# Performance work log

Hardware: AMD Instinct MI355X
Metric: run time of the kernel (lower is better)

The kernel has to match this reference:

```python
import jax, jax.numpy as jnp
import numpy as np


def setup_inputs() -> dict:
    key = jax.random.key(0)
    ks = jax.random.split(key, 8)
    B, C, H, W = 4, 512, 64, 64
    C8 = C // 8
    return {
        "x": jax.random.normal(ks[0], (B, C, H, W), dtype=jnp.float32),
        "Wq": jax.random.normal(ks[1], (C8, C), dtype=jnp.float32) * 0.02,
        "bq": jax.random.normal(ks[2], (C8,), dtype=jnp.float32) * 0.02,
        "Wk": jax.random.normal(ks[3], (C8, C), dtype=jnp.float32) * 0.02,
        "bk": jax.random.normal(ks[4], (C8,), dtype=jnp.float32) * 0.02,
        "Wv": jax.random.normal(ks[5], (C, C), dtype=jnp.float32) * 0.02,
        "bv": jax.random.normal(ks[6], (C,), dtype=jnp.float32) * 0.02,
        "gamma": jax.random.normal(ks[7], (1,), dtype=jnp.float32),
    }


def reference(x, Wq, bq, Wk, bk, Wv, bv, gamma):
    B, C, H, W = x.shape
    N = H * W
    xf = x.reshape(B, C, N)  # 1x1 conv == per-position matmul over channels
    q = jnp.einsum('oc,bcn->bno', Wq, xf) + bq  # B, N, C//8  (proj_query^T)
    k = jnp.einsum('oc,bcn->bon', Wk, xf) + bk[None, :, None]  # B, C//8, N
    v = jnp.einsum('oc,bcn->bon', Wv, xf) + bv[None, :, None]  # B, C, N
    energy = jnp.einsum('bno,bom->bnm', q, k)  # B, N, N
    attention = jax.nn.softmax(energy, axis=-1)
    # out = bmm(proj_value, attention^T): out[:, :, n] = sum_m v[:, :, m] * att[n, m]
    out = jnp.einsum('bcm,bnm->bcn', v, attention).reshape(B, C, H, W)
    return gamma[0] * out + x
```

## Files before the change

### kernel.cpp

```cpp
#include <hip/hip_runtime.h>
#include <stdint.h>


typedef unsigned short u16;
typedef unsigned char u8;
typedef __attribute__((ext_vector_type(8))) short short8;
typedef __attribute__((ext_vector_type(4))) float f32x4;
typedef __attribute__((ext_vector_type(16))) float f32x16;
typedef __attribute__((ext_vector_type(4))) int i32x4;
typedef __attribute__((ext_vector_type(8))) int i32x8;

#define ASYNC16(gp, lp)                                                        \
  __builtin_amdgcn_global_load_lds(                                            \
      (__attribute__((address_space(1))) void*)(void*)(gp),                    \
      (__attribute__((address_space(3))) void*)(lp), 16, 0, 0)

#define WAIT_VM0 0x0F70
#define WAIT_VM4 0x0F74
#define WAIT_VM8 0x0F78

#define EXP_SHIFT 5.0f
#define EXP_CAP 57000.0f

__device__ __forceinline__ u16 f2bf(float f) {
  uint32_t u = __float_as_uint(f);
  u += 0x7FFFu + ((u >> 16) & 1u);
  return (u16)(u >> 16);
}

__device__ __forceinline__ u8 f2fp8(float f) {
  f = fminf(fmaxf(f, -440.f), 440.f);
  int r = __builtin_amdgcn_cvt_pk_fp8_f32(f, f, 0, false);
  return (u8)(r & 0xFF);
}

__global__ __launch_bounds__(256) void k_transpose(const float* __restrict__ x,
                                                   u16* __restrict__ xT) {
  __shared__ float tile[32][33];
  const int b = blockIdx.z;
  const int nb = blockIdx.x * 32;
  const int cb = blockIdx.y * 32;
  const int t = threadIdx.x;
  {
    const int nl = t & 31, c0 = t >> 5;
    const float* xp = x + ((size_t)b * 512 + cb) * 4096 + nb;
#pragma unroll
    for (int i = 0; i < 4; ++i) {
      const int cl = c0 + i * 8;
      tile[cl][nl] = xp[(size_t)cl * 4096 + nl];
    }
  }
  __syncthreads();
  {
    const int cl = t & 31, n0 = t >> 5;
    u16* xtp = xT + ((size_t)b * 4096 + nb) * 512 + cb;
#pragma unroll
    for (int i = 0; i < 4; ++i) {
      const int nl = n0 + i * 8;
      xtp[(size_t)nl * 512 + cl] = f2bf(tile[cl][nl]);
    }
  }
}

__global__ __launch_bounds__(256) void k_wcast(const float* __restrict__ Wq,
                                               const float* __restrict__ Wk,
                                               const float* __restrict__ Wv,
                                               u16* __restrict__ wqk,
                                               u16* __restrict__ wv) {
  const int idx = blockIdx.x * 256 + threadIdx.x;
  if (idx < 128 * 512) {
    const int r = idx >> 9, c = idx & 511;
    const float f = (r < 64) ? Wq[r * 512 + c] : Wk[(r - 64) * 512 + c];
    wqk[idx] = f2bf(f);
  } else {
    const int j = idx - 128 * 512;
    if (j < 512 * 512) wv[j] = f2bf(Wv[j]);
  }
}

__device__ __forceinline__ void gemm_bt_tile(const u16* __restrict__ A,
                                             const u16* __restrict__ B,
                                             const int K, const int rowA0,
                                             const int colB0, u16* smem,
                                             f32x4 acc[4][4]) {
  const int t = threadIdx.x;
  const int lane = t & 63, wave = t >> 6;
  const int quad = lane >> 4, l15 = lane & 15;
  const int wr = wave >> 1, wc = wave & 1;
  u16* As = smem;
  u16* Bs = smem + 8192;
  const f32x4 zero = {0.f, 0.f, 0.f, 0.f};
#pragma unroll
  for (int i = 0; i < 4; ++i)
#pragma unroll
    for (int j = 0; j < 4; ++j) acc[i][j] = zero;

  const int srow = t >> 3;
  const int c8 = (lane & 7) ^ (lane >> 3);
  const u16* ga = A + (size_t)(rowA0 + srow) * K + c8 * 8;
  const u16* gb = B + (size_t)(colB0 + srow) * K + c8 * 8;
  char* la = (char*)As + wave * 1024;
  char* lb = (char*)Bs + wave * 1024;
  const size_t rK32 = (size_t)32 * K;

  const int sw0 = (quad) ^ (l15 & 7);
  const int sw1 = (4 + quad) ^ (l15 & 7);

  for (int k0 = 0; k0 < K; k0 += 64) {
    ASYNC16(ga + k0, la);
    ASYNC16(ga + k0 + rK32, la + 4096);
    ASYNC16(ga + k0 + 2 * rK32, la + 8192);
    ASYNC16(ga + k0 + 3 * rK32, la + 12288);
    ASYNC16(gb + k0, lb);
    ASYNC16(gb + k0 + rK32, lb + 4096);
    ASYNC16(gb + k0 + 2 * rK32, lb + 8192);
    ASYNC16(gb + k0 + 3 * rK32, lb + 12288);
    __syncthreads();
#pragma unroll
    for (int s = 0; s < 2; ++s) {
      const int sw = s ? sw1 : sw0;
      short8 a[4], b[4];
#pragma unroll
      for (int i = 0; i < 4; ++i)
        a[i] = *(const short8*)(As + (wr * 64 + i * 16 + l15) * 64 + sw * 8);
#pragma unroll
      for (int j = 0; j < 4; ++j)
        b[j] = *(const short8*)(Bs + (wc * 64 + j * 16 + l15) * 64 + sw * 8);
#pragma unroll
      for (int i = 0; i < 4; ++i)
#pragma unroll
        for (int j = 0; j < 4; ++j)
          acc[i][j] = __builtin_amdgcn_mfma_f32_16x16x32_bf16(a[i], b[j],
                                                              acc[i][j], 0, 0, 0);
    }
    __syncthreads();
  }
}

__global__ __launch_bounds__(256) void k_proj_qk(const u16* __restrict__ xT,
                                                 const u16* __restrict__ wqk,
                                                 const float* __restrict__ bq,
                                                 const float* __restrict__ bk,
                                                 u16* __restrict__ q,
                                                 u16* __restrict__ kT) {
  __shared__ u16 smem[16384];
  const int b = blockIdx.z;
  const int rowA0 = blockIdx.x * 128;
  f32x4 acc[4][4];
  gemm_bt_tile(xT + (size_t)b * 4096 * 512, wqk, 512, rowA0, 0, smem, acc);
  const int t = threadIdx.x, lane = t & 63, wave = t >> 6;
  const int quad = lane >> 4, l15 = lane & 15;
  const int wr = wave >> 1, wc = wave & 1;
#pragma unroll
  for (int j = 0; j < 4; ++j) {
    const int col = wc * 64 + j * 16 + l15;
    const float bias = (col < 64) ? bq[col] : bk[col - 64];
#pragma unroll
    for (int i = 0; i < 4; ++i) {
#pragma unroll
      for (int r = 0; r < 4; ++r) {
        const int row = rowA0 + wr * 64 + i * 16 + quad * 4 + r;
        const float val = acc[i][j][r] + bias;
        if (col < 64)
          q[((size_t)b * 4096 + row) * 64 + col] = f2bf(val);
        else
          kT[((size_t)b * 4096 + row) * 64 + (col - 64)] = f2bf(val);
      }
    }
  }
}

__global__ __launch_bounds__(256) void k_proj_v(const u16* __restrict__ wv,
                                                const u16* __restrict__ xT,
                                                const float* __restrict__ bv,
                                                u8* __restrict__ v8) {
  __shared__ u16 smem[16384];
  const int b = blockIdx.z;
  const int rowA0 = blockIdx.x * 128;
  const int colB0 = blockIdx.y * 128;
  f32x4 acc[4][4];
  gemm_bt_tile(wv, xT + (size_t)b * 4096 * 512, 512, rowA0, colB0, smem, acc);
  const int t = threadIdx.x, lane = t & 63, wave = t >> 6;
  const int quad = lane >> 4, l15 = lane & 15;
  const int wr = wave >> 1, wc = wave & 1;
#pragma unroll
  for (int i = 0; i < 4; ++i) {
#pragma unroll
    for (int r = 0; r < 4; ++r) {
      const int row = rowA0 + wr * 64 + i * 16 + quad * 4 + r;
      const float bias = bv[row];
#pragma unroll
      for (int j = 0; j < 4; ++j) {
        const int col = colB0 + wc * 64 + j * 16 + l15;
        v8[((size_t)b * 512 + row) * 4096 + col] = f2fp8(acc[i][j][r] + bias);
      }
    }
  }
}

__global__ __launch_bounds__(256, 4) void k_attn(const u16* __restrict__ q,
                                                 const u16* __restrict__ kT,
                                                 u8* __restrict__ E8,
                                                 float* __restrict__ lpart) {
  __shared__ u16 qs[4][16 * 64];
  __shared__ u16 ks[2][128 * 64];

  const int t = threadIdx.x;
  const int l = t & 63;
  const int w = t >> 6;
  const int quad = l >> 4, l15 = l & 15;
  const int c8 = (l & 7) ^ (l >> 3);
  const int r8 = l >> 3;

  const int row0 = blockIdx.x * 64 + w * 16;
  const int mpart = blockIdx.y;
  const int b = blockIdx.z;
  const int m_base = mpart * 1024;

  const u16* qg = q + ((size_t)b * 4096 + row0) * 64 + (size_t)r8 * 64 + c8 * 8;
  const u16* kg = kT + ((size_t)b * 4096 + m_base + w * 32) * 64 +
                  (size_t)r8 * 64 + c8 * 8;

  char* qls = (char*)qs + w * 2048;
  char* kls0 = (char*)ks[0] + w * 4096;
  char* kls1 = (char*)ks[1] + w * 4096;

  ASYNC16(qg, qls);
  ASYNC16(qg + 512, qls + 1024);
#pragma unroll
  for (int i = 0; i < 4; ++i) ASYNC16(kg + i * 512, kls0 + i * 1024);
#pragma unroll
  for (int i = 0; i < 4; ++i) ASYNC16(kg + 8192 + i * 512, kls1 + i * 1024);

  __builtin_amdgcn_s_waitcnt(WAIT_VM8);

  const int sw0 = quad ^ (l15 & 7);
  const int sw1 = (4 + quad) ^ (l15 & 7);
  const u16* qsw = qs[w];
  const short8 af0 = *(const short8*)(qsw + l15 * 64 + sw0 * 8);
  const short8 af1 = *(const short8*)(qsw + l15 * 64 + sw1 * 8);

  float lsum = 0.f;
  u8* Ep = E8 + ((size_t)b * 4096 + row0 + l15) * 4096 + m_base + quad * 4;
  const f32x4 zero = {0.f, 0.f, 0.f, 0.f};

  for (int it = 0; it < 8; ++it) {
    if (it < 7)
      __builtin_amdgcn_s_waitcnt(WAIT_VM4);
    else
      __builtin_amdgcn_s_waitcnt(WAIT_VM0);
    __builtin_amdgcn_s_barrier();
    asm volatile("" ::: "memory");

    const u16* kb = ks[it & 1];
    f32x4 acc[8];
#pragma unroll
    for (int j = 0; j < 8; ++j) acc[j] = zero;
    __builtin_amdgcn_s_setprio(1);
#pragma unroll
    for (int j = 0; j < 8; ++j)
      acc[j] = __builtin_amdgcn_mfma_f32_16x16x32_bf16(
          *(const short8*)(kb + (j * 16 + l15) * 64 + sw0 * 8), af0, acc[j], 0, 0, 0);
#pragma unroll
    for (int j = 0; j < 8; ++j)
      acc[j] = __builtin_amdgcn_mfma_f32_16x16x32_bf16(
          *(const short8*)(kb + (j * 16 + l15) * 64 + sw1 * 8), af1, acc[j], 0, 0, 0);
    __builtin_amdgcn_s_setprio(0);
#pragma unroll
    for (int j = 0; j < 8; ++j) {
      const float e0 = fminf(__expf(acc[j][0] - EXP_SHIFT), EXP_CAP);
      const float e1 = fminf(__expf(acc[j][1] - EXP_SHIFT), EXP_CAP);
      const float e2 = fminf(__expf(acc[j][2] - EXP_SHIFT), EXP_CAP);
      const float e3 = fminf(__expf(acc[j][3] - EXP_SHIFT), EXP_CAP);
      lsum += (e0 + e1) + (e2 + e3);
      int pk = __builtin_amdgcn_cvt_pk_bf8_f32(e0, e1, 0, false);
      pk = __builtin_amdgcn_cvt_pk_bf8_f32(e2, e3, pk, true);
      *(int*)(Ep + it * 128 + j * 16) = pk;
    }

    asm volatile("" ::: "memory");
    __builtin_amdgcn_s_barrier();
    if (it < 6) {
      char* dst = (it & 1) ? kls1 : kls0;
      const u16* src = kg + (size_t)(it + 2) * 8192;
#pragma unroll
      for (int i = 0; i < 4; ++i) ASYNC16(src + i * 512, dst + i * 1024);
    }
  }

  lsum += __shfl_xor(lsum, 16);
  lsum += __shfl_xor(lsum, 32);
  if (l < 16)
    lpart[(size_t)mpart * 16384 + (size_t)b * 4096 + row0 + l] = lsum;
}

__global__ __launch_bounds__(256) void k_lsum(const float* __restrict__ lp,
                                              float* __restrict__ ilg) {
  const int i = blockIdx.x * 256 + threadIdx.x;
  ilg[i] = 1.0f / (lp[i] + lp[16384 + i] + lp[32768 + i] + lp[49152 + i]);
}

__global__ __launch_bounds__(256) void k_pv(const u8* __restrict__ v8,
                                            const u8* __restrict__ E8,
                                            const float* __restrict__ ilg,
                                            const float* __restrict__ x,
                                            const float* __restrict__ gamma,
                                            float* __restrict__ out) {
  __shared__ u8 As[4][8192];
  __shared__ u8 Bs[4][8192];
  const int bid = blockIdx.x;
  const int xcd = bid & 7;
  const int slot = bid >> 3;
  const int c_idx = slot >> 4;
  const int group = xcd * 16 + (slot & 15);
  const int b = group >> 5;
  const int n_idx = group & 31;
  const int rowA0 = c_idx * 128;
  const int colB0 = n_idx * 128;

  const u8* Ag = v8 + (size_t)b * 512 * 4096;
  const u8* Bg = E8 + (size_t)b * 4096 * 4096;

  const int t = threadIdx.x;
  const int l = t & 63, w = t >> 6;
  const int wr = w >> 1, wc = w & 1;
  const int l31 = l & 31, h = l >> 5;

  const int srow = w * 16 + (l >> 2);
  const int ca = l & 3;
  const int f0 = (srow >> 1) & 3;
  const int f1 = ((srow + 64) >> 1) & 3;
  const u8* gA0 = Ag + (size_t)(rowA0 + srow) * 4096 + (ca ^ f0) * 16;
  const u8* gA1 = Ag + (size_t)(rowA0 + srow + 64) * 4096 + (ca ^ f1) * 16;
  const u8* gB0 = Bg + (size_t)(colB0 + srow) * 4096 + (ca ^ f0) * 16;
  const u8* gB1 = Bg + (size_t)(colB0 + srow + 64) * 4096 + (ca ^ f1) * 16;

#define STAGE_PV(bi, k0)                                                       \
  do {                                                                         \
    char* la_ = (char*)As[bi] + w * 1024;                                      \
    char* lb_ = (char*)Bs[bi] + w * 1024;                                      \
    ASYNC16(gA0 + (k0), la_);                                                  \
    ASYNC16(gA1 + (k0), la_ + 4096);                                           \
    ASYNC16(gB0 + (k0), lb_);                                                  \
    ASYNC16(gB1 + (k0), lb_ + 4096);                                           \
  } while (0)

  int rowA[2], rowB[2], sA1[2], sA2[2], sB1[2], sB2[2];
#pragma unroll
  for (int i = 0; i < 2; ++i) {
    rowA[i] = wr * 64 + i * 32 + l31;
    const int fa = (rowA[i] >> 1) & 3;
    sA1[i] = (2 * h) ^ fa;
    sA2[i] = (2 * h + 1) ^ fa;
    rowB[i] = wc * 64 + i * 32 + l31;
    const int fb = (rowB[i] >> 1) & 3;
    sB1[i] = (2 * h) ^ fb;
    sB2[i] = (2 * h + 1) ^ fb;
  }

  f32x16 acc[2][2];
#pragma unroll
  for (int i = 0; i < 2; ++i)
#pragma unroll
    for (int j = 0; j < 2; ++j)
#pragma unroll
      for (int r = 0; r < 16; ++r) acc[i][j][r] = 0.f;

  STAGE_PV(0, 0);
  STAGE_PV(1, 64);

  for (int it = 0; it < 64; ++it) {
    if (it < 63)
      __builtin_amdgcn_s_waitcnt(WAIT_VM4);
    else
      __builtin_amdgcn_s_waitcnt(WAIT_VM0);
    asm volatile("" ::: "memory");
    __builtin_amdgcn_s_barrier();
    asm volatile("" ::: "memory");
    if (it + 2 < 64) STAGE_PV((it + 2) & 3, (it + 2) * 64);

    const u8* Asb = As[it & 3];
    const u8* Bsb = Bs[it & 3];
    i32x8 a[2], bb[2];
#pragma unroll
    for (int i = 0; i < 2; ++i) {
      const u8* pa = Asb + rowA[i] * 64;
      const i32x4 lo = *(const i32x4*)(pa + sA1[i] * 16);
      const i32x4 hi = *(const i32x4*)(pa + sA2[i] * 16);
      a[i][0] = lo[0]; a[i][1] = lo[1]; a[i][2] = lo[2]; a[i][3] = lo[3];
      a[i][4] = hi[0]; a[i][5] = hi[1]; a[i][6] = hi[2]; a[i][7] = hi[3];
      const u8* pb = Bsb + rowB[i] * 64;
      const i32x4 blo = *(const i32x4*)(pb + sB1[i] * 16);
      const i32x4 bhi = *(const i32x4*)(pb + sB2[i] * 16);
      bb[i][0] = blo[0]; bb[i][1] = blo[1]; bb[i][2] = blo[2]; bb[i][3] = blo[3];
      bb[i][4] = bhi[0]; bb[i][5] = bhi[1]; bb[i][6] = bhi[2]; bb[i][7] = bhi[3];
    }
    __builtin_amdgcn_s_setprio(1);
#pragma unroll
    for (int i = 0; i < 2; ++i)
#pragma unroll
      for (int j = 0; j < 2; ++j)
        acc[i][j] = __builtin_amdgcn_mfma_scale_f32_32x32x64_f8f6f4(
            a[i], bb[j], acc[i][j], 0 , 1 , 0, 0x7F, 0, 0x7F);
    __builtin_amdgcn_s_setprio(0);
    asm volatile("" ::: "memory");
  }
#undef STAGE_PV

  const float g = gamma[0];
#pragma unroll
  for (int j = 0; j < 2; ++j) {
    const int col = colB0 + wc * 64 + j * 32 + l31;
    const float gil = g * ilg[(size_t)b * 4096 + col];
#pragma unroll
    for (int i = 0; i < 2; ++i) {
#pragma unroll
      for (int r = 0; r < 16; ++r) {
        const int rloc = (r & 3) + 8 * (r >> 2) + 4 * h;
        const int row = rowA0 + wr * 64 + i * 32 + rloc;
        const size_t idx = ((size_t)b * 512 + row) * 4096 + col;
        out[idx] = gil * acc[i][j][r] + x[idx];
      }
    }
  }
}

extern "C" void kernel_launch(void* const* d_in, const int* in_sizes, int n_in,
                              void* d_out, int out_size, void* d_ws,
                              size_t ws_size, hipStream_t stream) {
  const float* x = (const float*)d_in[0];
  const float* Wq = (const float*)d_in[1];
  const float* bq = (const float*)d_in[2];
  const float* Wk = (const float*)d_in[3];
  const float* bk = (const float*)d_in[4];
  const float* Wv = (const float*)d_in[5];
  const float* bv = (const float*)d_in[6];
  const float* gamma = (const float*)d_in[7];
  float* out = (float*)d_out;

  char* ws = (char*)d_ws;
  u16* xT = (u16*)(ws);
  u16* wqk = (u16*)(ws + 16777216);
  u16* wv = (u16*)(ws + 16908288);
  u16* qb = (u16*)(ws + 17432576);
  u16* ktb = (u16*)(ws + 19529728);
  u8* v8 = (u8*)(ws + 21626880);
  u8* E8 = (u8*)(ws + 30015488);
  float* lpart = (float*)(ws + 97124352);
  float* ilg = (float*)(ws + 97386496);

  k_transpose<<<dim3(128, 16, 4), 256, 0, stream>>>(x, xT);
  k_wcast<<<dim3(1280), 256, 0, stream>>>(Wq, Wk, Wv, wqk, wv);
  k_proj_qk<<<dim3(32, 1, 4), 256, 0, stream>>>(xT, wqk, bq, bk, qb, ktb);
  k_proj_v<<<dim3(4, 32, 4), 256, 0, stream>>>(wv, xT, bv, v8);
  k_attn<<<dim3(64, 4, 4), 256, 0, stream>>>(qb, ktb, E8, lpart);
  k_lsum<<<dim3(64), 256, 0, stream>>>(lpart, ilg);
  k_pv<<<dim3(512), 256, 0, stream>>>(v8, E8, ilg, x, gamma, out);
}
```

Measured before the change: 213.2 us.

## Use 8 waves per block in PV kernel and deepen async prefetch to three stages

```diff
diff --git a/kernel.cpp b/kernel.cpp
--- a/kernel.cpp
+++ b/kernel.cpp
@@ -16,6 +16,7 @@
       (__attribute__((address_space(3))) void*)(lp), 16, 0, 0)
 
 #define WAIT_VM0 0x0F70
+#define WAIT_VM2 0x0F72
 #define WAIT_VM4 0x0F74
 #define WAIT_VM8 0x0F78
 
@@ -300,12 +301,12 @@
   ilg[i] = 1.0f / (lp[i] + lp[16384 + i] + lp[32768 + i] + lp[49152 + i]);
 }
 
-__global__ __launch_bounds__(256) void k_pv(const u8* __restrict__ v8,
-                                            const u8* __restrict__ E8,
-                                            const float* __restrict__ ilg,
-                                            const float* __restrict__ x,
-                                            const float* __restrict__ gamma,
-                                            float* __restrict__ out) {
+__global__ __launch_bounds__(512, 4) void k_pv(const u8* __restrict__ v8,
+                                               const u8* __restrict__ E8,
+                                               const float* __restrict__ ilg,
+                                               const float* __restrict__ x,
+                                               const float* __restrict__ gamma,
+                                               float* __restrict__ out) {
   __shared__ u8 As[4][8192];
   __shared__ u8 Bs[4][8192];
   const int bid = blockIdx.x;
@@ -323,65 +324,59 @@
 
   const int t = threadIdx.x;
   const int l = t & 63, w = t >> 6;
-  const int wr = w >> 1, wc = w & 1;
+  const int wr = w >> 2, wc = w & 3;
   const int l31 = l & 31, h = l >> 5;
 
   const int srow = w * 16 + (l >> 2);
   const int ca = l & 3;
-  const int f0 = (srow >> 1) & 3;
-  const int f1 = ((srow + 64) >> 1) & 3;
-  const u8* gA0 = Ag + (size_t)(rowA0 + srow) * 4096 + (ca ^ f0) * 16;
-  const u8* gA1 = Ag + (size_t)(rowA0 + srow + 64) * 4096 + (ca ^ f1) * 16;
-  const u8* gB0 = Bg + (size_t)(colB0 + srow) * 4096 + (ca ^ f0) * 16;
-  const u8* gB1 = Bg + (size_t)(colB0 + srow + 64) * 4096 + (ca ^ f1) * 16;
+  const int fs = (srow >> 1) & 3;
+  const u8* gA = Ag + (size_t)(rowA0 + srow) * 4096 + (ca ^ fs) * 16;
+  const u8* gB = Bg + (size_t)(colB0 + srow) * 4096 + (ca ^ fs) * 16;
 
 #define STAGE_PV(bi, k0)                                                       \
   do {                                                                         \
-    char* la_ = (char*)As[bi] + w * 1024;                                      \
-    char* lb_ = (char*)Bs[bi] + w * 1024;                                      \
-    ASYNC16(gA0 + (k0), la_);                                                  \
-    ASYNC16(gA1 + (k0), la_ + 4096);                                           \
-    ASYNC16(gB0 + (k0), lb_);                                                  \
-    ASYNC16(gB1 + (k0), lb_ + 4096);                                           \
+    ASYNC16(gA + (k0), (char*)As[bi] + w * 1024);                              \
+    ASYNC16(gB + (k0), (char*)Bs[bi] + w * 1024);                              \
   } while (0)
 
-  int rowA[2], rowB[2], sA1[2], sA2[2], sB1[2], sB2[2];
+  int rowA[2], sA1[2], sA2[2];
 #pragma unroll
   for (int i = 0; i < 2; ++i) {
     rowA[i] = wr * 64 + i * 32 + l31;
     const int fa = (rowA[i] >> 1) & 3;
     sA1[i] = (2 * h) ^ fa;
     sA2[i] = (2 * h + 1) ^ fa;
-    rowB[i] = wc * 64 + i * 32 + l31;
-    const int fb = (rowB[i] >> 1) & 3;
-    sB1[i] = (2 * h) ^ fb;
-    sB2[i] = (2 * h + 1) ^ fb;
-  }
-
-  f32x16 acc[2][2];
+  }
+  const int rowB = wc * 32 + l31;
+  const int fb = (rowB >> 1) & 3;
+  const int sB1 = (2 * h) ^ fb;
+  const int sB2 = (2 * h + 1) ^ fb;
+
+  f32x16 acc[2];
 #pragma unroll
   for (int i = 0; i < 2; ++i)
 #pragma unroll
-    for (int j = 0; j < 2; ++j)
-#pragma unroll
-      for (int r = 0; r < 16; ++r) acc[i][j][r] = 0.f;
+    for (int r = 0; r < 16; ++r) acc[i][r] = 0.f;
 
   STAGE_PV(0, 0);
   STAGE_PV(1, 64);
+  STAGE_PV(2, 128);
 
   for (int it = 0; it < 64; ++it) {
-    if (it < 63)
+    if (it < 62)
       __builtin_amdgcn_s_waitcnt(WAIT_VM4);
+    else if (it == 62)
+      __builtin_amdgcn_s_waitcnt(WAIT_VM2);
     else
       __builtin_amdgcn_s_waitcnt(WAIT_VM0);
     asm volatile("" ::: "memory");
     __builtin_amdgcn_s_barrier();
     asm volatile("" ::: "memory");
-    if (it + 2 < 64) STAGE_PV((it + 2) & 3, (it + 2) * 64);
+    if (it + 3 < 64) STAGE_PV((it + 3) & 3, (it + 3) * 64);
 
     const u8* Asb = As[it & 3];
     const u8* Bsb = Bs[it & 3];
-    i32x8 a[2], bb[2];
+    i32x8 a[2], bb;
 #pragma unroll
     for (int i = 0; i < 2; ++i) {
       const u8* pa = Asb + rowA[i] * 64;
@@ -389,38 +384,35 @@
       const i32x4 hi = *(const i32x4*)(pa + sA2[i] * 16);
       a[i][0] = lo[0]; a[i][1] = lo[1]; a[i][2] = lo[2]; a[i][3] = lo[3];
       a[i][4] = hi[0]; a[i][5] = hi[1]; a[i][6] = hi[2]; a[i][7] = hi[3];
-      const u8* pb = Bsb + rowB[i] * 64;
-      const i32x4 blo = *(const i32x4*)(pb + sB1[i] * 16);
-      const i32x4 bhi = *(const i32x4*)(pb + sB2[i] * 16);
-      bb[i][0] = blo[0]; bb[i][1] = blo[1]; bb[i][2] = blo[2]; bb[i][3] = blo[3];
-      bb[i][4] = bhi[0]; bb[i][5] = bhi[1]; bb[i][6] = bhi[2]; bb[i][7] = bhi[3];
+    }
+    {
+      const u8* pb = Bsb + rowB * 64;
+      const i32x4 blo = *(const i32x4*)(pb + sB1 * 16);
+      const i32x4 bhi = *(const i32x4*)(pb + sB2 * 16);
+      bb[0] = blo[0]; bb[1] = blo[1]; bb[2] = blo[2]; bb[3] = blo[3];
+      bb[4] = bhi[0]; bb[5] = bhi[1]; bb[6] = bhi[2]; bb[7] = bhi[3];
     }
     __builtin_amdgcn_s_setprio(1);
 #pragma unroll
     for (int i = 0; i < 2; ++i)
-#pragma unroll
-      for (int j = 0; j < 2; ++j)
-        acc[i][j] = __builtin_amdgcn_mfma_scale_f32_32x32x64_f8f6f4(
-            a[i], bb[j], acc[i][j], 0 , 1 , 0, 0x7F, 0, 0x7F);
+      acc[i] = __builtin_amdgcn_mfma_scale_f32_32x32x64_f8f6f4(
+          a[i], bb, acc[i], 0 , 1 , 0, 0x7F, 0, 0x7F);
     __builtin_amdgcn_s_setprio(0);
     asm volatile("" ::: "memory");
   }
 #undef STAGE_PV
 
   const float g = gamma[0];
-#pragma unroll
-  for (int j = 0; j < 2; ++j) {
-    const int col = colB0 + wc * 64 + j * 32 + l31;
-    const float gil = g * ilg[(size_t)b * 4096 + col];
-#pragma unroll
-    for (int i = 0; i < 2; ++i) {
-#pragma unroll
-      for (int r = 0; r < 16; ++r) {
-        const int rloc = (r & 3) + 8 * (r >> 2) + 4 * h;
-        const int row = rowA0 + wr * 64 + i * 32 + rloc;
-        const size_t idx = ((size_t)b * 512 + row) * 4096 + col;
-        out[idx] = gil * acc[i][j][r] + x[idx];
-      }
+  const int col = colB0 + wc * 32 + l31;
+  const float gil = g * ilg[(size_t)b * 4096 + col];
+#pragma unroll
+  for (int i = 0; i < 2; ++i) {
+#pragma unroll
+    for (int r = 0; r < 16; ++r) {
+      const int rloc = (r & 3) + 8 * (r >> 2) + 4 * h;
+      const int row = rowA0 + wr * 64 + i * 32 + rloc;
+      const size_t idx = ((size_t)b * 512 + row) * 4096 + col;
+      out[idx] = gil * acc[i][r] + x[idx];
     }
   }
 }
@@ -455,5 +447,5 @@
   k_proj_v<<<dim3(4, 32, 4), 256, 0, stream>>>(wv, xT, bv, v8);
   k_attn<<<dim3(64, 4, 4), 256, 0, stream>>>(qb, ktb, E8, lpart);
   k_lsum<<<dim3(64), 256, 0, stream>>>(lpart, ilg);
-  k_pv<<<dim3(512), 256, 0, stream>>>(v8, E8, ilg, x, gamma, out);
-}
+  k_pv<<<dim3(512), 512, 0, stream>>>(v8, E8, ilg, x, gamma, out);
+}
```

New measurement: 210.2 us. Within noise of the previous version (-1.4%).

## Enlarge PV GEMM tile to 256x256 with 512 threads and deeper prefetch

Applied to the files above, without the earlier changes.

```diff
diff --git a/kernel.cpp b/kernel.cpp
--- a/kernel.cpp
+++ b/kernel.cpp
@@ -300,67 +300,70 @@
   ilg[i] = 1.0f / (lp[i] + lp[16384 + i] + lp[32768 + i] + lp[49152 + i]);
 }
 
-__global__ __launch_bounds__(256) void k_pv(const u8* __restrict__ v8,
-                                            const u8* __restrict__ E8,
-                                            const float* __restrict__ ilg,
-                                            const float* __restrict__ x,
-                                            const float* __restrict__ gamma,
-                                            float* __restrict__ out) {
-  __shared__ u8 As[4][8192];
-  __shared__ u8 Bs[4][8192];
+__global__ __launch_bounds__(512, 2) void k_pv(const u8* __restrict__ v8,
+                                               const u8* __restrict__ E8,
+                                               const float* __restrict__ ilg,
+                                               const float* __restrict__ x,
+                                               const float* __restrict__ gamma,
+                                               float* __restrict__ out) {
+  __shared__ u8 As[4][16384];
+  __shared__ u8 Bs[4][16384];
   const int bid = blockIdx.x;
   const int xcd = bid & 7;
   const int slot = bid >> 3;
-  const int c_idx = slot >> 4;
-  const int group = xcd * 16 + (slot & 15);
-  const int b = group >> 5;
-  const int n_idx = group & 31;
-  const int rowA0 = c_idx * 128;
-  const int colB0 = n_idx * 128;
+  const int c_idx = slot & 1;
+  const int group = xcd * 8 + (slot >> 1);
+  const int b = group >> 4;
+  const int n_idx = group & 15;
+  const int rowA0 = c_idx * 256;
+  const int colB0 = n_idx * 256;
 
   const u8* Ag = v8 + (size_t)b * 512 * 4096;
   const u8* Bg = E8 + (size_t)b * 4096 * 4096;
 
   const int t = threadIdx.x;
   const int l = t & 63, w = t >> 6;
-  const int wr = w >> 1, wc = w & 1;
+  const int wr = w >> 2, wc = w & 3;
   const int l31 = l & 31, h = l >> 5;
 
-  const int srow = w * 16 + (l >> 2);
-  const int ca = l & 3;
-  const int f0 = (srow >> 1) & 3;
-  const int f1 = ((srow + 64) >> 1) & 3;
-  const u8* gA0 = Ag + (size_t)(rowA0 + srow) * 4096 + (ca ^ f0) * 16;
-  const u8* gA1 = Ag + (size_t)(rowA0 + srow + 64) * 4096 + (ca ^ f1) * 16;
-  const u8* gB0 = Bg + (size_t)(colB0 + srow) * 4096 + (ca ^ f0) * 16;
-  const u8* gB1 = Bg + (size_t)(colB0 + srow + 64) * 4096 + (ca ^ f1) * 16;
+  const int srow0 = t >> 2;
+  const int srow1 = srow0 + 128;
+  const int ca = t & 3;
+  const int f0 = (srow0 >> 1) & 3;
+  const int f1 = (srow1 >> 1) & 3;
+  const u8* gA0 = Ag + (size_t)(rowA0 + srow0) * 4096 + (ca ^ f0) * 16;
+  const u8* gA1 = Ag + (size_t)(rowA0 + srow1) * 4096 + (ca ^ f1) * 16;
+  const u8* gB0 = Bg + (size_t)(colB0 + srow0) * 4096 + (ca ^ f0) * 16;
+  const u8* gB1 = Bg + (size_t)(colB0 + srow1) * 4096 + (ca ^ f1) * 16;
 
 #define STAGE_PV(bi, k0)                                                       \
   do {                                                                         \
-    char* la_ = (char*)As[bi] + w * 1024;                                      \
-    char* lb_ = (char*)Bs[bi] + w * 1024;                                      \
-    ASYNC16(gA0 + (k0), la_);                                                  \
-    ASYNC16(gA1 + (k0), la_ + 4096);                                           \
-    ASYNC16(gB0 + (k0), lb_);                                                  \
-    ASYNC16(gB1 + (k0), lb_ + 4096);                                           \
+    ASYNC16(gA0 + (k0), (char*)As[bi] + w * 1024);                             \
+    ASYNC16(gA1 + (k0), (char*)As[bi] + 8192 + w * 1024);                      \
+    ASYNC16(gB0 + (k0), (char*)Bs[bi] + w * 1024);                             \
+    ASYNC16(gB1 + (k0), (char*)Bs[bi] + 8192 + w * 1024);                      \
   } while (0)
 
-  int rowA[2], rowB[2], sA1[2], sA2[2], sB1[2], sB2[2];
-#pragma unroll
-  for (int i = 0; i < 2; ++i) {
-    rowA[i] = wr * 64 + i * 32 + l31;
+  int rowA[4], sA1[4], sA2[4];
+#pragma unroll
+  for (int i = 0; i < 4; ++i) {
+    rowA[i] = wr * 128 + i * 32 + l31;
     const int fa = (rowA[i] >> 1) & 3;
     sA1[i] = (2 * h) ^ fa;
     sA2[i] = (2 * h + 1) ^ fa;
-    rowB[i] = wc * 64 + i * 32 + l31;
-    const int fb = (rowB[i] >> 1) & 3;
-    sB1[i] = (2 * h) ^ fb;
-    sB2[i] = (2 * h + 1) ^ fb;
-  }
-
-  f32x16 acc[2][2];
-#pragma unroll
-  for (int i = 0; i < 2; ++i)
+  }
+  int rowB[2], sB1[2], sB2[2];
+#pragma unroll
+  for (int j = 0; j < 2; ++j) {
+    rowB[j] = wc * 64 + j * 32 + l31;
+    const int fb = (rowB[j] >> 1) & 3;
+    sB1[j] = (2 * h) ^ fb;
+    sB2[j] = (2 * h + 1) ^ fb;
+  }
+
+  f32x16 acc[4][2];
+#pragma unroll
+  for (int i = 0; i < 4; ++i)
 #pragma unroll
     for (int j = 0; j < 2; ++j)
 #pragma unroll
@@ -368,36 +371,42 @@
 
   STAGE_PV(0, 0);
   STAGE_PV(1, 64);
+  STAGE_PV(2, 128);
 
   for (int it = 0; it < 64; ++it) {
-    if (it < 63)
+    if (it < 62)
+      __builtin_amdgcn_s_waitcnt(WAIT_VM8);
+    else if (it == 62)
       __builtin_amdgcn_s_waitcnt(WAIT_VM4);
     else
       __builtin_amdgcn_s_waitcnt(WAIT_VM0);
     asm volatile("" ::: "memory");
     __builtin_amdgcn_s_barrier();
     asm volatile("" ::: "memory");
-    if (it + 2 < 64) STAGE_PV((it + 2) & 3, (it + 2) * 64);
+    if (it + 3 < 64) STAGE_PV((it + 3) & 3, (it + 3) * 64);
 
     const u8* Asb = As[it & 3];
     const u8* Bsb = Bs[it & 3];
-    i32x8 a[2], bb[2];
-#pragma unroll
-    for (int i = 0; i < 2; ++i) {
+    i32x8 a[4], bb[2];
+#pragma unroll
+    for (int i = 0; i < 4; ++i) {
       const u8* pa = Asb + rowA[i] * 64;
       const i32x4 lo = *(const i32x4*)(pa + sA1[i] * 16);
       const i32x4 hi = *(const i32x4*)(pa + sA2[i] * 16);
       a[i][0] = lo[0]; a[i][1] = lo[1]; a[i][2] = lo[2]; a[i][3] = lo[3];
       a[i][4] = hi[0]; a[i][5] = hi[1]; a[i][6] = hi[2]; a[i][7] = hi[3];
-      const u8* pb = Bsb + rowB[i] * 64;
-      const i32x4 blo = *(const i32x4*)(pb + sB1[i] * 16);
-      const i32x4 bhi = *(const i32x4*)(pb + sB2[i] * 16);
-      bb[i][0] = blo[0]; bb[i][1] = blo[1]; bb[i][2] = blo[2]; bb[i][3] = blo[3];
-      bb[i][4] = bhi[0]; bb[i][5] = bhi[1]; bb[i][6] = bhi[2]; bb[i][7] = bhi[3];
+    }
+#pragma unroll
+    for (int j = 0; j < 2; ++j) {
+      const u8* pb = Bsb + rowB[j] * 64;
+      const i32x4 blo = *(const i32x4*)(pb + sB1[j] * 16);
+      const i32x4 bhi = *(const i32x4*)(pb + sB2[j] * 16);
+      bb[j][0] = blo[0]; bb[j][1] = blo[1]; bb[j][2] = blo[2]; bb[j][3] = blo[3];
+      bb[j][4] = bhi[0]; bb[j][5] = bhi[1]; bb[j][6] = bhi[2]; bb[j][7] = bhi[3];
     }
     __builtin_amdgcn_s_setprio(1);
 #pragma unroll
-    for (int i = 0; i < 2; ++i)
+    for (int i = 0; i < 4; ++i)
 #pragma unroll
       for (int j = 0; j < 2; ++j)
         acc[i][j] = __builtin_amdgcn_mfma_scale_f32_32x32x64_f8f6f4(
@@ -413,11 +422,11 @@
     const int col = colB0 + wc * 64 + j * 32 + l31;
     const float gil = g * ilg[(size_t)b * 4096 + col];
 #pragma unroll
-    for (int i = 0; i < 2; ++i) {
+    for (int i = 0; i < 4; ++i) {
 #pragma unroll
       for (int r = 0; r < 16; ++r) {
         const int rloc = (r & 3) + 8 * (r >> 2) + 4 * h;
-        const int row = rowA0 + wr * 64 + i * 32 + rloc;
+        const int row = rowA0 + wr * 128 + i * 32 + rloc;
         const size_t idx = ((size_t)b * 512 + row) * 4096 + col;
         out[idx] = gil * acc[i][j][r] + x[idx];
       }
@@ -455,5 +464,5 @@
   k_proj_v<<<dim3(4, 32, 4), 256, 0, stream>>>(wv, xT, bv, v8);
   k_attn<<<dim3(64, 4, 4), 256, 0, stream>>>(qb, ktb, E8, lpart);
   k_lsum<<<dim3(64), 256, 0, stream>>>(lpart, ilg);
-  k_pv<<<dim3(512), 256, 0, stream>>>(v8, E8, ilg, x, gamma, out);
-}
+  k_pv<<<dim3(128), 512, 0, stream>>>(v8, E8, ilg, x, gamma, out);
+}
```

Measured after the change: 232.7 us. +9.1%, slower.
